# Performance work log

Hardware: AMD Instinct MI355X
Metric: run time of the kernel (lower is better)

## Reference

```python
import jax, jax.numpy as jnp
import numpy as np

N = 50000          # nodes
E = 1600000        # edges (avg degree 32)
G = 16             # graphs in batch
H = 128            # hidden_dim
HOP = 3
IN_DIM = 1


def setup_inputs() -> dict:
    key = jax.random.key(0)
    ks = jax.random.split(key, 12)
    s = 1.0 / np.sqrt(H)
    return {
        "x": jax.random.normal(ks[0], (N, IN_DIM), jnp.float32),
        "edge_index": jax.random.randint(ks[1], (2, E), 0, N, jnp.int64),
        "edge_attr": jax.random.uniform(ks[2], (E, 1), jnp.float32),
        "batch": jnp.sort(jax.random.randint(ks[3], (N,), 0, G, jnp.int64)),
        "W1": jax.random.normal(ks[4], (HOP, H, IN_DIM), jnp.float32) * s,
        "W2": jax.random.normal(ks[5], (HOP, H, H), jnp.float32) * s,
        "W3": jax.random.normal(ks[6], (HOP, H, H), jnp.float32) * s,
        "W4": jax.random.normal(ks[7], (HOP, H, 1), jnp.float32) * s,
        "W5": jax.random.normal(ks[8], (1, 2 * H), jnp.float32) * s,
        "b5": jnp.zeros((1,), jnp.float32),
        "W6": jax.random.normal(ks[9], (H, H), jnp.float32) * s,
        "W7": jax.random.normal(ks[10], (H, H), jnp.float32) * s,
    }


def reference(x, edge_index, edge_attr, batch, W1, W2, W3, W4, W5, b5, W6, W7):
    row, col = edge_index[0], edge_index[1]
    node_emb = jnp.zeros((N, H), x.dtype)
    for l in range(HOP):
        nfe = x @ W1[l].T                                        # [N,H]
        # gather neighbor embeddings along col, scatter-add to row
        ne_aggr = jax.ops.segment_sum(node_emb[col], row, num_segments=N)
        efe = jax.nn.relu(edge_attr @ W4[l].T)                   # [E,H]
        ee_aggr = jax.ops.segment_sum(efe, row, num_segments=N)  # [N,H]
        node_emb = jax.nn.relu(nfe + ne_aggr @ W2[l].T + ee_aggr @ W3[l].T)
    pooled = jax.ops.segment_sum(node_emb, batch, num_segments=G)  # [G,H]
    sum_emb = pooled @ W6.T                                        # [G,H]
    cat = jax.nn.relu(jnp.concatenate([sum_emb[batch], node_emb @ W7.T], axis=-1))
    return cat @ W5.T + b5                                         # [N,1]
```

## Files before the change

kernel.cpp:

```cpp
#include <hip/hip_runtime.h>
#include <hip/hip_bf16.h>

#define N_NODES 50000
#define N_EDGES 1600000
#define NGRAPH  16
#define HID     128

#define RPB   128
#define NB    ((N_NODES + RPB - 1) / RPB)
#define NBLK  256
#define EPB   ((N_EDGES + NBLK - 1) / NBLK)

typedef unsigned int uint32;
typedef unsigned short ushort;
typedef unsigned char uchar;
typedef __attribute__((ext_vector_type(8))) short bf16x8;
typedef __attribute__((ext_vector_type(4))) float f32x4;
typedef __attribute__((ext_vector_type(2))) float f32x2;

__device__ __forceinline__ uint32 bf16r(float f) {
    uint32 b = __float_as_uint(f);
    return (b + 0x7fffu + ((b >> 16) & 1u)) >> 16;
}
__device__ __forceinline__ uint32 pack_bf16(float lo, float hi) {
    return bf16r(lo) | (bf16r(hi) << 16);
}
__device__ __forceinline__ float bf_lo(uint32 u) { return __uint_as_float(u << 16); }
__device__ __forceinline__ float bf_hi(uint32 u) { return __uint_as_float(u & 0xffff0000u); }

__global__ __launch_bounds__(256) void k_init(float* p, int n,
                                              const int* __restrict__ batch,
                                              int* __restrict__ gstart) {
    int i = blockIdx.x * 256 + threadIdx.x;
    if (i < n) p[i] = 0.f;
    if (i <= NGRAPH) {
        int lo = 0, hi = N_NODES;
        while (lo < hi) {
            int mid = (lo + hi) >> 1;
            if (batch[mid] < i) lo = mid + 1; else hi = mid;
        }
        gstart[i] = lo;
    }
}

__global__ __launch_bounds__(1024) void k_p1_hist(const int* __restrict__ row,
                                                  int* __restrict__ blkhist) {
    __shared__ int hist[NB];
    int tid = threadIdx.x, blk = blockIdx.x;
    for (int i = tid; i < NB; i += 1024) hist[i] = 0;
    __syncthreads();
    int s = blk * EPB, e = s + EPB; if (e > N_EDGES) e = N_EDGES;
    for (int i = s + tid; i < e; i += 1024)
        atomicAdd(&hist[row[i] >> 7], 1);
    __syncthreads();
    for (int i = tid; i < NB; i += 1024)
        blkhist[i * NBLK + blk] = hist[i];
}

__global__ __launch_bounds__(NBLK) void k_p2a(int* __restrict__ blkhist,
                                              int* __restrict__ btot) {
    __shared__ int sums[NBLK];
    int t = threadIdx.x, b = blockIdx.x;
    int v = blkhist[b * NBLK + t];
    sums[t] = v;
    __syncthreads();
    for (int d = 1; d < NBLK; d <<= 1) {
        int u = (t >= d) ? sums[t - d] : 0;
        __syncthreads();
        sums[t] += u;
        __syncthreads();
    }
    blkhist[b * NBLK + t] = sums[t] - v;
    if (t == NBLK - 1) btot[b] = sums[t];
}

__global__ __launch_bounds__(512) void k_p2b(const int* __restrict__ btot,
                                             int* __restrict__ bbase) {
    __shared__ int sums[512];
    int t = threadIdx.x;
    int s = (t < NB) ? btot[t] : 0;
    sums[t] = s;
    __syncthreads();
    for (int d = 1; d < 512; d <<= 1) {
        int v = (t >= d) ? sums[t - d] : 0;
        __syncthreads();
        sums[t] += v;
        __syncthreads();
    }
    if (t < NB) {
        bbase[t] = sums[t] - s;
        if (t == NB - 1) bbase[NB] = sums[t];
    }
}

__global__ __launch_bounds__(1024) void k_p3_part(const int* __restrict__ row,
                                                  const int* __restrict__ col,
                                                  const float* __restrict__ ea,
                                                  const int* __restrict__ blkhist,
                                                  const int* __restrict__ bbase,
                                                  int2* __restrict__ pea) {
    __shared__ int cur[NB];
    int tid = threadIdx.x, blk = blockIdx.x;
    for (int i = tid; i < NB; i += 1024)
        cur[i] = bbase[i] + blkhist[i * NBLK + blk];
    __syncthreads();
    int s = blk * EPB, e = s + EPB; if (e > N_EDGES) e = N_EDGES;
    for (int i = s + tid; i < e; i += 1024) {
        int r = row[i], c = col[i];
        float a = ea[i];
        int slot = atomicAdd(&cur[r >> 7], 1);
        pea[slot] = make_int2(((r & (RPB - 1)) << 16) | c, __float_as_int(a));
    }
}

__global__ __launch_bounds__(512) void k_p4a(const int2* __restrict__ pea,
                                             const int* __restrict__ bbase,
                                             const float* __restrict__ x,
                                             int* __restrict__ offs,
                                             float* __restrict__ ea_sum,
                                             float2* __restrict__ pxe) {
    __shared__ int   cnt[RPB];
    __shared__ float eas[RPB];
    __shared__ int   scan_s[RPB];
    int tid = threadIdx.x, b = blockIdx.x;
    if (tid < RPB) { cnt[tid] = 0; eas[tid] = 0.f; }
    __syncthreads();
    int s = bbase[b], e = bbase[b + 1];
    for (int i = s + tid; i < e; i += 512) {
        int2 p = pea[i];
        int lr = ((uint32)p.x) >> 16;
        atomicAdd(&cnt[lr], 1);
        atomicAdd(&eas[lr], __int_as_float(p.y));
    }
    __syncthreads();
    if (tid < RPB) scan_s[tid] = cnt[tid];
    __syncthreads();
    for (int d = 1; d < RPB; d <<= 1) {
        int v = 0;
        if (tid < RPB && tid >= d) v = scan_s[tid - d];
        __syncthreads();
        if (tid < RPB) scan_s[tid] += v;
        __syncthreads();
    }
    int nbase = b * RPB;
    if (tid < RPB) {
        int excl = scan_s[tid] - cnt[tid];
        int n = nbase + tid;
        if (n < N_NODES) {
            offs[n] = s + excl;
            ea_sum[n] = eas[tid];
            pxe[n] = make_float2(x[n], eas[tid]);
        }
    }
    if (b == NB - 1 && tid == 0) offs[N_NODES] = e;
}

__global__ __launch_bounds__(512) void k_p4b(const int2* __restrict__ pea,
                                             const int* __restrict__ bbase,
                                             const int* __restrict__ offs,
                                             const float2* __restrict__ pxe,
                                             int* __restrict__ csr,
                                             float2* __restrict__ pxec) {
    __shared__ int cur[RPB];
    int tid = threadIdx.x, b = blockIdx.x;
    int nbase = b * RPB;
    if (tid < RPB) cur[tid] = (nbase + tid < N_NODES) ? offs[nbase + tid] : 0;
    __syncthreads();
    int s = bbase[b], e = bbase[b + 1];
    for (int i = s + tid; i < e; i += 512) {
        int2 p = pea[i];
        int c = p.x & 0xFFFF;
        int slot = atomicAdd(&cur[((uint32)p.x) >> 16], 1);
        csr[slot] = c;
        pxec[slot] = pxe[c];
    }
}

__global__ __launch_bounds__(256) void k_prep(const float* __restrict__ W2,
                                              const float* __restrict__ W7,
                                              const float* __restrict__ W3,
                                              const float* __restrict__ W4,
                                              ushort* __restrict__ wpack,
                                              float* __restrict__ v3) {
    int idx = blockIdx.x * 256 + threadIdx.x;
    if (idx < 4 * 16384) {
        int m = idx >> 14, f = idx & 16383;
        int j = f & 7, lane = (f >> 3) & 63, kk = (f >> 9) & 3, t = (f >> 11) & 7;
        int hp = t * 16 + (lane & 15);
        int k  = kk * 32 + ((lane >> 4) & 3) * 8 + j;
        const float* src = (m < 3) ? (W2 + m * HID * HID) : W7;
        wpack[idx] = (ushort)bf16r(src[hp * HID + k]);
    }
    if (idx < 3 * HID) {
        int l = idx / HID, hp = idx % HID;
        float acc = 0.f;
        for (int h = 0; h < HID; h++)
            acc += W3[l * HID * HID + hp * HID + h] * fmaxf(W4[l * HID + h], 0.f);
        v3[idx] = acc;
    }
}

__global__ __launch_bounds__(256) void k_gather1(const float2* __restrict__ pxec,
                                                 const int* __restrict__ offs,
                                                 const float* __restrict__ w1,
                                                 const float* __restrict__ v3,
                                                 uint32* __restrict__ agg) {
    int node = (blockIdx.x * 256 + threadIdx.x) >> 6;
    int lane = threadIdx.x & 63;
    if (node >= N_NODES) return;
    f32x2 w1v = {w1[2 * lane], w1[2 * lane + 1]};
    f32x2 v3v = {v3[2 * lane], v3[2 * lane + 1]};
    const f32x2 zero = {0.f, 0.f};
    int s = offs[node], e = offs[node + 1];
    f32x2 acc[4] = {zero, zero, zero, zero};
    int j = s;
    for (; j + 8 <= e; j += 8) {
        float2 p[8];
#pragma unroll
        for (int u = 0; u < 8; u++) p[u] = pxec[j + u];
#pragma unroll
        for (int u = 0; u < 8; u++) {
            f32x2 px = {p[u].x, p[u].x};
            f32x2 pe = {p[u].y, p[u].y};
            f32x2 r = __builtin_elementwise_fma(px, w1v, pe * v3v);
            acc[u & 3] += __builtin_elementwise_max(r, zero);
        }
    }
    for (; j < e; j++) {
        float2 p = pxec[j];
        f32x2 px = {p.x, p.x};
        f32x2 pe = {p.y, p.y};
        f32x2 r = __builtin_elementwise_fma(px, w1v, pe * v3v);
        acc[0] += __builtin_elementwise_max(r, zero);
    }
    f32x2 rs = (acc[0] + acc[1]) + (acc[2] + acc[3]);
    agg[(size_t)node * 64 + lane] = pack_bf16(rs.x, rs.y);
}

__global__ __launch_bounds__(256) void k_gather(const uchar* __restrict__ emb8,
                                                const int* __restrict__ offs,
                                                const int* __restrict__ csr,
                                                uint32* __restrict__ agg) {
    int node = (blockIdx.x * 256 + threadIdx.x) >> 6;
    int lane = threadIdx.x & 63;
    if (node >= N_NODES) return;
    int s = offs[node], e = offs[node + 1];
    float ax[8] = {0.f}, ay[8] = {0.f};
    for (int base = s; base < e; base += 64) {
        int idx = base + lane;
        int cv = (idx < e) ? csr[idx] : 0;
        int cnt = e - base; if (cnt > 64) cnt = 64;
        int j = 0;
        for (; j + 8 <= cnt; j += 8) {
            int h16[8];
#pragma unroll
            for (int u = 0; u < 8; u++) {
                int c = __shfl(cv, j + u);
                h16[u] = *(const ushort*)(emb8 + (size_t)c * 128 + 2 * lane);
            }
#pragma unroll
            for (int u = 0; u < 8; u++) {
                f32x2 d = __builtin_amdgcn_cvt_pk_f32_fp8(h16[u], false);
                ax[u] += d.x; ay[u] += d.y;
            }
        }
        for (; j < cnt; j++) {
            int c = __shfl(cv, j);
            int h = *(const ushort*)(emb8 + (size_t)c * 128 + 2 * lane);
            f32x2 d = __builtin_amdgcn_cvt_pk_f32_fp8(h, false);
            ax[0] += d.x; ay[0] += d.y;
        }
    }
    float rx = (((ax[0] + ax[1]) + (ax[2] + ax[3])) + ((ax[4] + ax[5]) + (ax[6] + ax[7]))) * 64.f;
    float ry = (((ay[0] + ay[1]) + (ay[2] + ay[3])) + ((ay[4] + ay[5]) + (ay[6] + ay[7]))) * 64.f;
    agg[(size_t)node * 64 + lane] = pack_bf16(rx, ry);
}

#define LROW 136

template <bool LAST>
__global__ __launch_bounds__(256) void k_gemm(const uint32* __restrict__ agg,
                                              const ushort* __restrict__ w2p,
                                              const float* __restrict__ w1l,
                                              const float* __restrict__ v3l,
                                              const float* __restrict__ x,
                                              const float* __restrict__ ea_sum,
                                              uint32* __restrict__ embOut,
                                              uchar* __restrict__ emb8Out,
                                              const ushort* __restrict__ w7p,
                                              const float* __restrict__ W5,
                                              float* __restrict__ outp) {
    __shared__ ushort tile[64 * LROW];
    int tid = threadIdx.x;
    int tbase = blockIdx.x * 64;
    {
        const uint2* src = (const uint2*)(agg + (size_t)tbase * 64);
        int vn = N_NODES - tbase; if (vn > 64) vn = 64;
        int lim = vn * 32;
        for (int i = tid; i < 64 * 32; i += 256) {
            uint2 u = (i < lim) ? src[i] : make_uint2(0u, 0u);
            int r = i >> 5, c4 = (i & 31) * 4;
            *(uint2*)&tile[r * LROW + c4] = u;
        }
    }
    __syncthreads();
    int wv = tid >> 6, lane = tid & 63;
    int n0 = lane & 15, quad = lane >> 4;
    int arow = wv * 16 + n0;
    bf16x8 a0 = *(const bf16x8*)&tile[arow * LROW + 0 * 32 + quad * 8];
    bf16x8 a1 = *(const bf16x8*)&tile[arow * LROW + 1 * 32 + quad * 8];
    bf16x8 a2 = *(const bf16x8*)&tile[arow * LROW + 2 * 32 + quad * 8];
    bf16x8 a3 = *(const bf16x8*)&tile[arow * LROW + 3 * 32 + quad * 8];
    const bf16x8* wb = (const bf16x8*)w2p;
    f32x4 acc[8];
#pragma unroll
    for (int t = 0; t < 8; t++) {
        f32x4 c = {0.f, 0.f, 0.f, 0.f};
        c = __builtin_amdgcn_mfma_f32_16x16x32_bf16(a0, wb[(t * 4 + 0) * 64 + lane], c, 0, 0, 0);
        c = __builtin_amdgcn_mfma_f32_16x16x32_bf16(a1, wb[(t * 4 + 1) * 64 + lane], c, 0, 0, 0);
        c = __builtin_amdgcn_mfma_f32_16x16x32_bf16(a2, wb[(t * 4 + 2) * 64 + lane], c, 0, 0, 0);
        c = __builtin_amdgcn_mfma_f32_16x16x32_bf16(a3, wb[(t * 4 + 3) * 64 + lane], c, 0, 0, 0);
        acc[t] = c;
    }
    float xs[4], es[4];
#pragma unroll
    for (int r = 0; r < 4; r++) {
        int n = tbase + wv * 16 + quad * 4 + r;
        xs[r] = (n < N_NODES) ? x[n] : 0.f;
        es[r] = (n < N_NODES) ? ea_sum[n] : 0.f;
    }
    if (!LAST) {
        uchar* stile = (uchar*)tile;
#pragma unroll
        for (int t = 0; t < 8; t++) {
            int hp = t * 16 + n0;
            float w1v = w1l[hp], v3v = v3l[hp];
#pragma unroll
            for (int r = 0; r < 4; r++) {
                float v = fmaxf(acc[t][r] + xs[r] * w1v + es[r] * v3v, 0.f) * 0.015625f;
                int enc = __builtin_amdgcn_cvt_pk_fp8_f32(v, v, 0, false);
                stile[(wv * 16 + quad * 4 + r) * 136 + hp] = (uchar)(enc & 0xff);
            }
        }
        __syncthreads();
        int vn = N_NODES - tbase; if (vn > 64) vn = 64;
        for (int i = tid; i < 64 * 32; i += 256) {
            int r = i >> 5, c4 = (i & 31) * 4;
            if (r < vn) {
                uint32 u = *(const uint32*)&stile[r * 136 + c4];
                *(uint32*)(emb8Out + (size_t)(tbase + r) * 128 + c4) = u;
            }
        }
    } else {
#pragma unroll
        for (int t = 0; t < 8; t++) {
            int hp = t * 16 + n0;
            float w1v = w1l[hp], v3v = v3l[hp];
#pragma unroll
            for (int r = 0; r < 4; r++) {
                float v = fmaxf(acc[t][r] + xs[r] * w1v + es[r] * v3v, 0.f);
                tile[(wv * 16 + quad * 4 + r) * LROW + hp] = (ushort)bf16r(v);
            }
        }
        __syncthreads();
        {
            int vn = N_NODES - tbase; if (vn > 64) vn = 64;
            for (int i = tid; i < 64 * 32; i += 256) {
                int r = i >> 5, c4 = (i & 31) * 4;
                if (r < vn) {
                    uint2 u = *(const uint2*)&tile[r * LROW + c4];
                    *(uint2*)(embOut + (size_t)(tbase + r) * 64 + (size_t)(i & 31) * 2) = u;
                }
            }
        }
        bf16x8 b0 = *(const bf16x8*)&tile[arow * LROW + 0 * 32 + quad * 8];
        bf16x8 b1 = *(const bf16x8*)&tile[arow * LROW + 1 * 32 + quad * 8];
        bf16x8 b2 = *(const bf16x8*)&tile[arow * LROW + 2 * 32 + quad * 8];
        bf16x8 b3 = *(const bf16x8*)&tile[arow * LROW + 3 * 32 + quad * 8];
        const bf16x8* w7 = (const bf16x8*)w7p;
        float p[4] = {0.f, 0.f, 0.f, 0.f};
#pragma unroll
        for (int t = 0; t < 8; t++) {
            f32x4 c = {0.f, 0.f, 0.f, 0.f};
            c = __builtin_amdgcn_mfma_f32_16x16x32_bf16(b0, w7[(t * 4 + 0) * 64 + lane], c, 0, 0, 0);
            c = __builtin_amdgcn_mfma_f32_16x16x32_bf16(b1, w7[(t * 4 + 1) * 64 + lane], c, 0, 0, 0);
            c = __builtin_amdgcn_mfma_f32_16x16x32_bf16(b2, w7[(t * 4 + 2) * 64 + lane], c, 0, 0, 0);
            c = __builtin_amdgcn_mfma_f32_16x16x32_bf16(b3, w7[(t * 4 + 3) * 64 + lane], c, 0, 0, 0);
            float w5v = W5[128 + t * 16 + n0];
#pragma unroll
            for (int r = 0; r < 4; r++) p[r] += fmaxf(c[r], 0.f) * w5v;
        }
#pragma unroll
        for (int r = 0; r < 4; r++) {
            float v = p[r];
            v += __shfl_xor(v, 1);
            v += __shfl_xor(v, 2);
            v += __shfl_xor(v, 4);
            v += __shfl_xor(v, 8);
            int n = tbase + wv * 16 + quad * 4 + r;
            if (n0 == 0 && n < N_NODES) outp[n] = v;
        }
    }
}

__global__ __launch_bounds__(256) void k_pool2(const uint32* __restrict__ emb,
                                               const int* __restrict__ gstart,
                                               float* __restrict__ pooled) {
    __shared__ float2 red[4][64];
    int bid = blockIdx.x;
    int g = bid >> 4, chunk = bid & 15;
    int gs = gstart[g], ge = gstart[g + 1];
    int len = ge - gs;
    int cs = gs + (int)(((long long)len * chunk) >> 4);
    int ce = gs + (int)(((long long)len * (chunk + 1)) >> 4);
    int sub = threadIdx.x >> 6, lane = threadIdx.x & 63;
    float ax = 0.f, ay = 0.f;
    for (int n = cs + sub; n < ce; n += 4) {
        uint32 u = emb[(size_t)n * 64 + lane];
        ax += bf_lo(u); ay += bf_hi(u);
    }
    red[sub][lane] = make_float2(ax, ay);
    __syncthreads();
    if (sub == 0) {
        float2 r0 = red[0][lane], r1 = red[1][lane], r2 = red[2][lane], r3 = red[3][lane];
        atomicAdd(&pooled[g * HID + 2 * lane],     (r0.x + r1.x) + (r2.x + r3.x));
        atomicAdd(&pooled[g * HID + 2 * lane + 1], (r0.y + r1.y) + (r2.y + r3.y));
    }
}

__global__ __launch_bounds__(128) void k_graph(const float* __restrict__ pooled,
                                               const float* __restrict__ W6,
                                               const float* __restrict__ W5,
                                               float* __restrict__ s_g) {
    int g = blockIdx.x, hp = threadIdx.x;
    float acc = 0.f;
    for (int h = 0; h < HID; h++) acc += pooled[g * HID + h] * W6[hp * HID + h];
    float v = fmaxf(acc, 0.f) * W5[hp];
    __shared__ float red[HID];
    red[hp] = v;
    __syncthreads();
    for (int d = 64; d > 0; d >>= 1) {
        if (hp < d) red[hp] += red[hp + d];
        __syncthreads();
    }
    if (hp == 0) s_g[g] = red[0];
}

__global__ __launch_bounds__(256) void k_addsg(float* __restrict__ out,
                                               const int* __restrict__ batch,
                                               const float* __restrict__ s_g,
                                               const float* __restrict__ b5) {
    int n = blockIdx.x * 256 + threadIdx.x;
    if (n < N_NODES) out[n] += s_g[batch[n]] + b5[0];
}

extern "C" void kernel_launch(void* const* d_in, const int* in_sizes, int n_in,
                              void* d_out, int out_size, void* d_ws, size_t ws_size,
                              hipStream_t stream) {
    (void)in_sizes; (void)n_in; (void)out_size; (void)ws_size;
    const float* x    = (const float*)d_in[0];
    const int*   ei   = (const int*)d_in[1];
    const float* ea   = (const float*)d_in[2];
    const int*   bat  = (const int*)d_in[3];
    const float* W1   = (const float*)d_in[4];
    const float* W2   = (const float*)d_in[5];
    const float* W3   = (const float*)d_in[6];
    const float* W4   = (const float*)d_in[7];
    const float* W5   = (const float*)d_in[8];
    const float* b5   = (const float*)d_in[9];
    const float* W6   = (const float*)d_in[10];
    const float* W7   = (const float*)d_in[11];
    float* out = (float*)d_out;

    const int* row = ei;
    const int* col = ei + N_EDGES;

    float* wsf = (float*)d_ws;
    int*   wsi = (int*)d_ws;
    size_t o = 0;
    float* pooled = wsf + o; o += NGRAPH * HID;
    float* s_g    = wsf + o; o += NGRAPH;
    size_t ztot = o;
    int*   offs   = wsi + o; o += N_NODES + 1;
    float* ea_sum = wsf + o; o += N_NODES;
    int*   gstart = wsi + o; o += NGRAPH + 1;
    int*   btot   = wsi + o; o += NB;
    int*   bbase  = wsi + o; o += NB + 1;
    float* v3     = wsf + o; o += 3 * HID;
    int*   blkh   = wsi + o; o += NB * NBLK;
    o = (o + 1) & ~(size_t)1;
    float2* pxe   = (float2*)(wsi + o); o += 2 * (size_t)N_NODES;
    o = (o + 3) & ~(size_t)3;
    ushort* wpack = (ushort*)(wsi + o); o += 4 * 16384 / 2;
    int*    csr   = wsi + o; o += N_EDGES;
    o = (o + 1) & ~(size_t)1;
    int2*   pea   = (int2*)(wsi + o); o += 2 * (size_t)N_EDGES;
    float2* pxec  = (float2*)(wsi + o); o += 2 * (size_t)N_EDGES;
    o = (o + 1) & ~(size_t)1;
    uint32* embA  = (uint32*)(wsi + o); o += (size_t)N_NODES * 64;
    uchar*  emb8  = (uchar*)(wsi + o);  o += (size_t)N_NODES * 32;
    uint32* aggB  = (uint32*)(wsi + o); o += (size_t)N_NODES * 64;

    const ushort* w2p1 = wpack + 1 * 16384;
    const ushort* w2p2 = wpack + 2 * 16384;
    const ushort* w7p  = wpack + 3 * 16384;

    k_init<<<(int)((ztot + 255) / 256), 256, 0, stream>>>((float*)d_ws, (int)ztot, bat, gstart);
    k_p1_hist<<<NBLK, 1024, 0, stream>>>(row, blkh);
    k_p2a<<<NB, NBLK, 0, stream>>>(blkh, btot);
    k_p2b<<<1, 512, 0, stream>>>(btot, bbase);
    k_p3_part<<<NBLK, 1024, 0, stream>>>(row, col, ea, blkh, bbase, pea);
    k_p4a<<<NB, 512, 0, stream>>>(pea, bbase, x, offs, ea_sum, pxe);
    k_p4b<<<NB, 512, 0, stream>>>(pea, bbase, offs, pxe, csr, pxec);
    k_prep<<<(4 * 16384 + 255) / 256, 256, 0, stream>>>(W2, W7, W3, W4, (ushort*)wpack, v3);
    k_gather1<<<(N_NODES * 64 + 255) / 256, 256, 0, stream>>>(pxec, offs, W1, v3, aggB);
    k_gemm<false><<<(N_NODES + 63) / 64, 256, 0, stream>>>(
        aggB, w2p1, W1 + 1 * HID, v3 + 1 * HID, x, ea_sum, nullptr, emb8, nullptr, nullptr, nullptr);
    k_gather<<<(N_NODES * 64 + 255) / 256, 256, 0, stream>>>(emb8, offs, csr, aggB);
    k_gemm<true><<<(N_NODES + 63) / 64, 256, 0, stream>>>(
        aggB, w2p2, W1 + 2 * HID, v3 + 2 * HID, x, ea_sum, embA, nullptr, w7p, W5, out);
    k_pool2<<<NGRAPH * 16, 256, 0, stream>>>(embA, gstart, pooled);
    k_graph<<<NGRAPH, 128, 0, stream>>>(pooled, W6, W5, s_g);
    k_addsg<<<(N_NODES + 255) / 256, 256, 0, stream>>>(out, bat, s_g, b5);
}
```

Baseline: 281.8 us.

## Fuse preprocessing and tail kernels, pool inside final GEMM, drop pxec buffer

Merges zero-init with weight packing, folds the top-level bucket scan into the partition kernel, and merges the two per-bucket CSR passes into one kernel that caches edges in LDS. The first gather now reads node features through the CSR index instead of a pre-gathered per-edge array, so the 12.8MB pxec buffer is no longer written. The final GEMM accumulates graph pooling directly through atomics, so the bf16 embedding no longer round-trips to memory. Graph readout and bias addition move into one tail kernel that recomputes per-graph scalars in each block. The cost is redundant per-block prefix reductions, atomic contention on pooled sums, and an indirect gather in layer one.

```diff
diff --git a/kernel.cpp b/kernel.cpp
--- a/kernel.cpp
+++ b/kernel.cpp
@@ -10,6 +10,7 @@
 #define NB    ((N_NODES + RPB - 1) / RPB)
 #define NBLK  256
 #define EPB   ((N_EDGES + NBLK - 1) / NBLK)
+#define P4CAP 6144
 
 typedef unsigned int uint32;
 typedef unsigned short ushort;
@@ -25,164 +26,16 @@
 __device__ __forceinline__ uint32 pack_bf16(float lo, float hi) {
     return bf16r(lo) | (bf16r(hi) << 16);
 }
-__device__ __forceinline__ float bf_lo(uint32 u) { return __uint_as_float(u << 16); }
-__device__ __forceinline__ float bf_hi(uint32 u) { return __uint_as_float(u & 0xffff0000u); }
-
-__global__ __launch_bounds__(256) void k_init(float* p, int n,
-                                              const int* __restrict__ batch,
-                                              int* __restrict__ gstart) {
-    int i = blockIdx.x * 256 + threadIdx.x;
-    if (i < n) p[i] = 0.f;
-    if (i <= NGRAPH) {
-        int lo = 0, hi = N_NODES;
-        while (lo < hi) {
-            int mid = (lo + hi) >> 1;
-            if (batch[mid] < i) lo = mid + 1; else hi = mid;
-        }
-        gstart[i] = lo;
-    }
-}
-
-__global__ __launch_bounds__(1024) void k_p1_hist(const int* __restrict__ row,
-                                                  int* __restrict__ blkhist) {
-    __shared__ int hist[NB];
-    int tid = threadIdx.x, blk = blockIdx.x;
-    for (int i = tid; i < NB; i += 1024) hist[i] = 0;
-    __syncthreads();
-    int s = blk * EPB, e = s + EPB; if (e > N_EDGES) e = N_EDGES;
-    for (int i = s + tid; i < e; i += 1024)
-        atomicAdd(&hist[row[i] >> 7], 1);
-    __syncthreads();
-    for (int i = tid; i < NB; i += 1024)
-        blkhist[i * NBLK + blk] = hist[i];
-}
-
-__global__ __launch_bounds__(NBLK) void k_p2a(int* __restrict__ blkhist,
-                                              int* __restrict__ btot) {
-    __shared__ int sums[NBLK];
-    int t = threadIdx.x, b = blockIdx.x;
-    int v = blkhist[b * NBLK + t];
-    sums[t] = v;
-    __syncthreads();
-    for (int d = 1; d < NBLK; d <<= 1) {
-        int u = (t >= d) ? sums[t - d] : 0;
-        __syncthreads();
-        sums[t] += u;
-        __syncthreads();
-    }
-    blkhist[b * NBLK + t] = sums[t] - v;
-    if (t == NBLK - 1) btot[b] = sums[t];
-}
-
-__global__ __launch_bounds__(512) void k_p2b(const int* __restrict__ btot,
-                                             int* __restrict__ bbase) {
-    __shared__ int sums[512];
-    int t = threadIdx.x;
-    int s = (t < NB) ? btot[t] : 0;
-    sums[t] = s;
-    __syncthreads();
-    for (int d = 1; d < 512; d <<= 1) {
-        int v = (t >= d) ? sums[t - d] : 0;
-        __syncthreads();
-        sums[t] += v;
-        __syncthreads();
-    }
-    if (t < NB) {
-        bbase[t] = sums[t] - s;
-        if (t == NB - 1) bbase[NB] = sums[t];
-    }
-}
-
-__global__ __launch_bounds__(1024) void k_p3_part(const int* __restrict__ row,
-                                                  const int* __restrict__ col,
-                                                  const float* __restrict__ ea,
-                                                  const int* __restrict__ blkhist,
-                                                  const int* __restrict__ bbase,
-                                                  int2* __restrict__ pea) {
-    __shared__ int cur[NB];
-    int tid = threadIdx.x, blk = blockIdx.x;
-    for (int i = tid; i < NB; i += 1024)
-        cur[i] = bbase[i] + blkhist[i * NBLK + blk];
-    __syncthreads();
-    int s = blk * EPB, e = s + EPB; if (e > N_EDGES) e = N_EDGES;
-    for (int i = s + tid; i < e; i += 1024) {
-        int r = row[i], c = col[i];
-        float a = ea[i];
-        int slot = atomicAdd(&cur[r >> 7], 1);
-        pea[slot] = make_int2(((r & (RPB - 1)) << 16) | c, __float_as_int(a));
-    }
-}
-
-__global__ __launch_bounds__(512) void k_p4a(const int2* __restrict__ pea,
-                                             const int* __restrict__ bbase,
-                                             const float* __restrict__ x,
-                                             int* __restrict__ offs,
-                                             float* __restrict__ ea_sum,
-                                             float2* __restrict__ pxe) {
-    __shared__ int   cnt[RPB];
-    __shared__ float eas[RPB];
-    __shared__ int   scan_s[RPB];
-    int tid = threadIdx.x, b = blockIdx.x;
-    if (tid < RPB) { cnt[tid] = 0; eas[tid] = 0.f; }
-    __syncthreads();
-    int s = bbase[b], e = bbase[b + 1];
-    for (int i = s + tid; i < e; i += 512) {
-        int2 p = pea[i];
-        int lr = ((uint32)p.x) >> 16;
-        atomicAdd(&cnt[lr], 1);
-        atomicAdd(&eas[lr], __int_as_float(p.y));
-    }
-    __syncthreads();
-    if (tid < RPB) scan_s[tid] = cnt[tid];
-    __syncthreads();
-    for (int d = 1; d < RPB; d <<= 1) {
-        int v = 0;
-        if (tid < RPB && tid >= d) v = scan_s[tid - d];
-        __syncthreads();
-        if (tid < RPB) scan_s[tid] += v;
-        __syncthreads();
-    }
-    int nbase = b * RPB;
-    if (tid < RPB) {
-        int excl = scan_s[tid] - cnt[tid];
-        int n = nbase + tid;
-        if (n < N_NODES) {
-            offs[n] = s + excl;
-            ea_sum[n] = eas[tid];
-            pxe[n] = make_float2(x[n], eas[tid]);
-        }
-    }
-    if (b == NB - 1 && tid == 0) offs[N_NODES] = e;
-}
-
-__global__ __launch_bounds__(512) void k_p4b(const int2* __restrict__ pea,
-                                             const int* __restrict__ bbase,
-                                             const int* __restrict__ offs,
-                                             const float2* __restrict__ pxe,
-                                             int* __restrict__ csr,
-                                             float2* __restrict__ pxec) {
-    __shared__ int cur[RPB];
-    int tid = threadIdx.x, b = blockIdx.x;
-    int nbase = b * RPB;
-    if (tid < RPB) cur[tid] = (nbase + tid < N_NODES) ? offs[nbase + tid] : 0;
-    __syncthreads();
-    int s = bbase[b], e = bbase[b + 1];
-    for (int i = s + tid; i < e; i += 512) {
-        int2 p = pea[i];
-        int c = p.x & 0xFFFF;
-        int slot = atomicAdd(&cur[((uint32)p.x) >> 16], 1);
-        csr[slot] = c;
-        pxec[slot] = pxe[c];
-    }
-}
-
-__global__ __launch_bounds__(256) void k_prep(const float* __restrict__ W2,
+
+__global__ __launch_bounds__(256) void k_init(float* __restrict__ zp, int nz,
+                                              const float* __restrict__ W2,
                                               const float* __restrict__ W7,
                                               const float* __restrict__ W3,
                                               const float* __restrict__ W4,
                                               ushort* __restrict__ wpack,
                                               float* __restrict__ v3) {
     int idx = blockIdx.x * 256 + threadIdx.x;
+    if (idx < nz) zp[idx] = 0.f;
     if (idx < 4 * 16384) {
         int m = idx >> 14, f = idx & 16383;
         int j = f & 7, lane = (f >> 3) & 63, kk = (f >> 9) & 3, t = (f >> 11) & 7;
@@ -200,8 +53,133 @@
     }
 }
 
-__global__ __launch_bounds__(256) void k_gather1(const float2* __restrict__ pxec,
+__global__ __launch_bounds__(1024) void k_p1_hist(const int* __restrict__ row,
+                                                  int* __restrict__ blkhist) {
+    __shared__ int hist[NB];
+    int tid = threadIdx.x, blk = blockIdx.x;
+    for (int i = tid; i < NB; i += 1024) hist[i] = 0;
+    __syncthreads();
+    int s = blk * EPB, e = s + EPB; if (e > N_EDGES) e = N_EDGES;
+    for (int i = s + tid; i < e; i += 1024)
+        atomicAdd(&hist[row[i] >> 7], 1);
+    __syncthreads();
+    for (int i = tid; i < NB; i += 1024)
+        blkhist[i * NBLK + blk] = hist[i];
+}
+
+__global__ __launch_bounds__(NBLK) void k_p2a(int* __restrict__ blkhist,
+                                              int* __restrict__ btot) {
+    __shared__ int sums[NBLK];
+    int t = threadIdx.x, b = blockIdx.x;
+    int v = blkhist[b * NBLK + t];
+    sums[t] = v;
+    __syncthreads();
+    for (int d = 1; d < NBLK; d <<= 1) {
+        int u = (t >= d) ? sums[t - d] : 0;
+        __syncthreads();
+        sums[t] += u;
+        __syncthreads();
+    }
+    blkhist[b * NBLK + t] = sums[t] - v;
+    if (t == NBLK - 1) btot[b] = sums[t];
+}
+
+__global__ __launch_bounds__(1024) void k_p3_part(const int* __restrict__ row,
+                                                  const int* __restrict__ col,
+                                                  const float* __restrict__ ea,
+                                                  const int* __restrict__ blkhist,
+                                                  const int* __restrict__ btot,
+                                                  int2* __restrict__ pea) {
+    __shared__ int sc[512];
+    __shared__ int cur[NB];
+    int tid = threadIdx.x, blk = blockIdx.x;
+    if (tid < 512) sc[tid] = (tid < NB) ? btot[tid] : 0;
+    __syncthreads();
+    for (int d = 1; d < 512; d <<= 1) {
+        int v = 0;
+        if (tid < 512 && tid >= d) v = sc[tid - d];
+        __syncthreads();
+        if (tid < 512) sc[tid] += v;
+        __syncthreads();
+    }
+    for (int i = tid; i < NB; i += 1024)
+        cur[i] = (sc[i] - btot[i]) + blkhist[i * NBLK + blk];
+    __syncthreads();
+    int s = blk * EPB, e = s + EPB; if (e > N_EDGES) e = N_EDGES;
+    for (int i = s + tid; i < e; i += 1024) {
+        int r = row[i], c = col[i];
+        float a = ea[i];
+        int slot = atomicAdd(&cur[r >> 7], 1);
+        pea[slot] = make_int2(((r & (RPB - 1)) << 16) | c, __float_as_int(a));
+    }
+}
+
+__global__ __launch_bounds__(512) void k_p4(const int2* __restrict__ pea,
+                                            const int* __restrict__ btot,
+                                            const float* __restrict__ x,
+                                            int* __restrict__ offs,
+                                            float* __restrict__ ea_sum,
+                                            float2* __restrict__ pxe,
+                                            int* __restrict__ csr) {
+    __shared__ int2  cache[P4CAP];
+    __shared__ int   red[512];
+    __shared__ int   cnt[RPB];
+    __shared__ float eas[RPB];
+    __shared__ int   scan_s[RPB];
+    __shared__ int   curp[RPB];
+    int t = threadIdx.x, b = blockIdx.x;
+    red[t] = (t < b) ? btot[t] : 0;
+    __syncthreads();
+    for (int d = 256; d > 0; d >>= 1) {
+        if (t < d) red[t] += red[t + d];
+        __syncthreads();
+    }
+    int s = red[0];
+    int e = s + btot[b];
+    int len = e - s;
+    int clen = len < P4CAP ? len : P4CAP;
+    for (int i = t; i < clen; i += 512) cache[i] = pea[s + i];
+    if (t < RPB) { cnt[t] = 0; eas[t] = 0.f; }
+    __syncthreads();
+    for (int i = t; i < len; i += 512) {
+        int2 p = (i < P4CAP) ? cache[i] : pea[s + i];
+        int lr = ((uint32)p.x) >> 16;
+        atomicAdd(&cnt[lr], 1);
+        atomicAdd(&eas[lr], __int_as_float(p.y));
+    }
+    __syncthreads();
+    if (t < RPB) scan_s[t] = cnt[t];
+    __syncthreads();
+    for (int d = 1; d < RPB; d <<= 1) {
+        int v = 0;
+        if (t < RPB && t >= d) v = scan_s[t - d];
+        __syncthreads();
+        if (t < RPB) scan_s[t] += v;
+        __syncthreads();
+    }
+    int nbase = b * RPB;
+    if (t < RPB) {
+        int excl = scan_s[t] - cnt[t];
+        int n = nbase + t;
+        if (n < N_NODES) {
+            offs[n] = s + excl;
+            ea_sum[n] = eas[t];
+            pxe[n] = make_float2(x[n], eas[t]);
+        }
+        curp[t] = s + excl;
+    }
+    if (b == NB - 1 && t == 0) offs[N_NODES] = e;
+    __syncthreads();
+    for (int i = t; i < len; i += 512) {
+        int2 p = (i < P4CAP) ? cache[i] : pea[s + i];
+        int slot = atomicAdd(&curp[((uint32)p.x) >> 16], 1);
+        csr[slot] = p.x & 0xFFFF;
+    }
+}
+
+__global__ __launch_bounds__(256) void k_gather1(const float2* __restrict__ pxe,
                                                  const int* __restrict__ offs,
+                                                 const int* __restrict__ csr,
                                                  const float* __restrict__ w1,
                                                  const float* __restrict__ v3,
                                                  uint32* __restrict__ agg) {
@@ -213,25 +191,30 @@
     const f32x2 zero = {0.f, 0.f};
     int s = offs[node], e = offs[node + 1];
     f32x2 acc[4] = {zero, zero, zero, zero};
-    int j = s;
-    for (; j + 8 <= e; j += 8) {
-        float2 p[8];
-#pragma unroll
-        for (int u = 0; u < 8; u++) p[u] = pxec[j + u];
-#pragma unroll
-        for (int u = 0; u < 8; u++) {
-            f32x2 px = {p[u].x, p[u].x};
-            f32x2 pe = {p[u].y, p[u].y};
+    for (int base = s; base < e; base += 64) {
+        int idx = base + lane;
+        int cv = (idx < e) ? csr[idx] : 0;
+        int cnt = e - base; if (cnt > 64) cnt = 64;
+        int j = 0;
+        for (; j + 8 <= cnt; j += 8) {
+            float2 p[8];
+#pragma unroll
+            for (int u = 0; u < 8; u++) p[u] = pxe[__shfl(cv, j + u)];
+#pragma unroll
+            for (int u = 0; u < 8; u++) {
+                f32x2 px = {p[u].x, p[u].x};
+                f32x2 pe = {p[u].y, p[u].y};
+                f32x2 r = __builtin_elementwise_fma(px, w1v, pe * v3v);
+                acc[u & 3] += __builtin_elementwise_max(r, zero);
+            }
+        }
+        for (; j < cnt; j++) {
+            float2 p = pxe[__shfl(cv, j)];
+            f32x2 px = {p.x, p.x};
+            f32x2 pe = {p.y, p.y};
             f32x2 r = __builtin_elementwise_fma(px, w1v, pe * v3v);
-            acc[u & 3] += __builtin_elementwise_max(r, zero);
-        }
-    }
-    for (; j < e; j++) {
-        float2 p = pxec[j];
-        f32x2 px = {p.x, p.x};
-        f32x2 pe = {p.y, p.y};
-        f32x2 r = __builtin_elementwise_fma(px, w1v, pe * v3v);
-        acc[0] += __builtin_elementwise_max(r, zero);
+            acc[0] += __builtin_elementwise_max(r, zero);
+        }
     }
     f32x2 rs = (acc[0] + acc[1]) + (acc[2] + acc[3]);
     agg[(size_t)node * 64 + lane] = pack_bf16(rs.x, rs.y);
@@ -285,32 +268,24 @@
                                               const float* __restrict__ v3l,
                                               const float* __restrict__ x,
                                               const float* __restrict__ ea_sum,
-                                              uint32* __restrict__ embOut,
                                               uchar* __restrict__ emb8Out,
                                               const ushort* __restrict__ w7p,
                                               const float* __restrict__ W5,
-                                              float* __restrict__ outp) {
+                                              float* __restrict__ outp,
+                                              const int* __restrict__ batch,
+                                              float* __restrict__ pooled) {
     __shared__ ushort tile[64 * LROW];
+    __shared__ float redp[4][128];
     int tid = threadIdx.x;
     int tbase = blockIdx.x * 64;
-    {
-        const uint2* src = (const uint2*)(agg + (size_t)tbase * 64);
-        int vn = N_NODES - tbase; if (vn > 64) vn = 64;
-        int lim = vn * 32;
-        for (int i = tid; i < 64 * 32; i += 256) {
-            uint2 u = (i < lim) ? src[i] : make_uint2(0u, 0u);
-            int r = i >> 5, c4 = (i & 31) * 4;
-            *(uint2*)&tile[r * LROW + c4] = u;
-        }
-    }
-    __syncthreads();
     int wv = tid >> 6, lane = tid & 63;
     int n0 = lane & 15, quad = lane >> 4;
     int arow = wv * 16 + n0;
-    bf16x8 a0 = *(const bf16x8*)&tile[arow * LROW + 0 * 32 + quad * 8];
-    bf16x8 a1 = *(const bf16x8*)&tile[arow * LROW + 1 * 32 + quad * 8];
-    bf16x8 a2 = *(const bf16x8*)&tile[arow * LROW + 2 * 32 + quad * 8];
-    bf16x8 a3 = *(const bf16x8*)&tile[arow * LROW + 3 * 32 + quad * 8];
+    bf16x8 a0 = {0,0,0,0,0,0,0,0}, a1 = a0, a2 = a0, a3 = a0;
+    if (tbase + arow < N_NODES) {
+        const bf16x8* ap = (const bf16x8*)(agg + (size_t)(tbase + arow) * 64);
+        a0 = ap[0 + quad]; a1 = ap[4 + quad]; a2 = ap[8 + quad]; a3 = ap[12 + quad];
+    }
     const bf16x8* wb = (const bf16x8*)w2p;
     f32x4 acc[8];
 #pragma unroll
@@ -352,26 +327,49 @@
             }
         }
     } else {
+        int nlast = tbase + 63; if (nlast > N_NODES - 1) nlast = N_NODES - 1;
+        int g0 = batch[tbase];
+        bool uni = (batch[nlast] == g0);
+        int gr[4];
+        if (!uni) {
+#pragma unroll
+            for (int r = 0; r < 4; r++) {
+                int n = tbase + wv * 16 + quad * 4 + r;
+                gr[r] = (n < N_NODES) ? batch[n] : 0;
+            }
+        }
+        float st[8];
 #pragma unroll
         for (int t = 0; t < 8; t++) {
             int hp = t * 16 + n0;
             float w1v = w1l[hp], v3v = v3l[hp];
+            float stt = 0.f;
 #pragma unroll
             for (int r = 0; r < 4; r++) {
                 float v = fmaxf(acc[t][r] + xs[r] * w1v + es[r] * v3v, 0.f);
                 tile[(wv * 16 + quad * 4 + r) * LROW + hp] = (ushort)bf16r(v);
-            }
-        }
-        __syncthreads();
-        {
-            int vn = N_NODES - tbase; if (vn > 64) vn = 64;
-            for (int i = tid; i < 64 * 32; i += 256) {
-                int r = i >> 5, c4 = (i & 31) * 4;
-                if (r < vn) {
-                    uint2 u = *(const uint2*)&tile[r * LROW + c4];
-                    *(uint2*)(embOut + (size_t)(tbase + r) * 64 + (size_t)(i & 31) * 2) = u;
+                if (uni) {
+                    stt += v;
+                } else {
+                    int n = tbase + wv * 16 + quad * 4 + r;
+                    if (n < N_NODES) atomicAdd(&pooled[gr[r] * HID + hp], v);
                 }
             }
+            st[t] = stt;
+        }
+        if (uni) {
+#pragma unroll
+            for (int t = 0; t < 8; t++) {
+                float v = st[t];
+                v += __shfl_xor(v, 16);
+                v += __shfl_xor(v, 32);
+                if (lane < 16) redp[wv][t * 16 + lane] = v;
+            }
+        }
+        __syncthreads();
+        if (uni && tid < 128) {
+            float sp = (redp[0][tid] + redp[1][tid]) + (redp[2][tid] + redp[3][tid]);
+            atomicAdd(&pooled[g0 * HID + tid], sp);
         }
         bf16x8 b0 = *(const bf16x8*)&tile[arow * LROW + 0 * 32 + quad * 8];
         bf16x8 b1 = *(const bf16x8*)&tile[arow * LROW + 1 * 32 + quad * 8];
@@ -403,55 +401,50 @@
     }
 }
 
-__global__ __launch_bounds__(256) void k_pool2(const uint32* __restrict__ emb,
-                                               const int* __restrict__ gstart,
-                                               float* __restrict__ pooled) {
-    __shared__ float2 red[4][64];
-    int bid = blockIdx.x;
-    int g = bid >> 4, chunk = bid & 15;
-    int gs = gstart[g], ge = gstart[g + 1];
-    int len = ge - gs;
-    int cs = gs + (int)(((long long)len * chunk) >> 4);
-    int ce = gs + (int)(((long long)len * (chunk + 1)) >> 4);
-    int sub = threadIdx.x >> 6, lane = threadIdx.x & 63;
-    float ax = 0.f, ay = 0.f;
-    for (int n = cs + sub; n < ce; n += 4) {
-        uint32 u = emb[(size_t)n * 64 + lane];
-        ax += bf_lo(u); ay += bf_hi(u);
-    }
-    red[sub][lane] = make_float2(ax, ay);
-    __syncthreads();
-    if (sub == 0) {
-        float2 r0 = red[0][lane], r1 = red[1][lane], r2 = red[2][lane], r3 = red[3][lane];
-        atomicAdd(&pooled[g * HID + 2 * lane],     (r0.x + r1.x) + (r2.x + r3.x));
-        atomicAdd(&pooled[g * HID + 2 * lane + 1], (r0.y + r1.y) + (r2.y + r3.y));
-    }
-}
-
-__global__ __launch_bounds__(128) void k_graph(const float* __restrict__ pooled,
-                                               const float* __restrict__ W6,
-                                               const float* __restrict__ W5,
-                                               float* __restrict__ s_g) {
-    int g = blockIdx.x, hp = threadIdx.x;
+__global__ __launch_bounds__(256) void k_tail(float* __restrict__ out,
+                                              const int* __restrict__ batch,
+                                              const float* __restrict__ pooled,
+                                              const float* __restrict__ W6,
+                                              const float* __restrict__ W5,
+                                              const float* __restrict__ b5) {
+    __shared__ float red[256];
+    __shared__ int gsh[2];
+    int t = threadIdx.x;
+    int nbase = blockIdx.x * 256;
+    int n = nbase + t;
+    if (t == 0) gsh[0] = batch[nbase < N_NODES ? nbase : N_NODES - 1];
+    if (t == 1) gsh[1] = batch[(nbase + 255) < N_NODES ? (nbase + 255) : N_NODES - 1];
+    __syncthreads();
+    int g_lo = gsh[0], g_hi = gsh[1];
+    int hp = t & 127;
+    int g = (t >> 7) ? g_hi : g_lo;
+    const float* pg = pooled + g * HID;
+    const float* wr = W6 + hp * HID;
     float acc = 0.f;
-    for (int h = 0; h < HID; h++) acc += pooled[g * HID + h] * W6[hp * HID + h];
-    float v = fmaxf(acc, 0.f) * W5[hp];
-    __shared__ float red[HID];
-    red[hp] = v;
+    for (int h = 0; h < HID; h++) acc += pg[h] * wr[h];
+    red[t] = fmaxf(acc, 0.f) * W5[hp];
     __syncthreads();
     for (int d = 64; d > 0; d >>= 1) {
-        if (hp < d) red[hp] += red[hp + d];
-        __syncthreads();
-    }
-    if (hp == 0) s_g[g] = red[0];
-}
-
-__global__ __launch_bounds__(256) void k_addsg(float* __restrict__ out,
-                                               const int* __restrict__ batch,
-                                               const float* __restrict__ s_g,
-                                               const float* __restrict__ b5) {
-    int n = blockIdx.x * 256 + threadIdx.x;
-    if (n < N_NODES) out[n] += s_g[batch[n]] + b5[0];
+        if (hp < d) red[t] += red[t + d];
+        __syncthreads();
+    }
+    float s_lo = red[0], s_hi = red[128];
+    if (n < N_NODES) {
+        int gn = batch[n];
+        float s;
+        if (gn == g_lo) s = s_lo;
+        else if (gn == g_hi) s = s_hi;
+        else {
+            s = 0.f;
+            const float* pg2 = pooled + gn * HID;
+            for (int hp2 = 0; hp2 < HID; hp2++) {
+                float a2 = 0.f;
+                for (int h = 0; h < HID; h++) a2 += pg2[h] * W6[hp2 * HID + h];
+                s += fmaxf(a2, 0.f) * W5[hp2];
+            }
+        }
+        out[n] += s + b5[0];
+    }
 }
 
 extern "C" void kernel_launch(void* const* d_in, const int* in_sizes, int n_in,
@@ -479,13 +472,10 @@
     int*   wsi = (int*)d_ws;
     size_t o = 0;
     float* pooled = wsf + o; o += NGRAPH * HID;
-    float* s_g    = wsf + o; o += NGRAPH;
     size_t ztot = o;
     int*   offs   = wsi + o; o += N_NODES + 1;
     float* ea_sum = wsf + o; o += N_NODES;
-    int*   gstart = wsi + o; o += NGRAPH + 1;
     int*   btot   = wsi + o; o += NB;
-    int*   bbase  = wsi + o; o += NB + 1;
     float* v3     = wsf + o; o += 3 * HID;
     int*   blkh   = wsi + o; o += NB * NBLK;
     o = (o + 1) & ~(size_t)1;
@@ -495,31 +485,25 @@
     int*    csr   = wsi + o; o += N_EDGES;
     o = (o + 1) & ~(size_t)1;
     int2*   pea   = (int2*)(wsi + o); o += 2 * (size_t)N_EDGES;
-    float2* pxec  = (float2*)(wsi + o); o += 2 * (size_t)N_EDGES;
-    o = (o + 1) & ~(size_t)1;
-    uint32* embA  = (uint32*)(wsi + o); o += (size_t)N_NODES * 64;
+    uint32* aggB  = (uint32*)(wsi + o); o += (size_t)N_NODES * 64;
     uchar*  emb8  = (uchar*)(wsi + o);  o += (size_t)N_NODES * 32;
-    uint32* aggB  = (uint32*)(wsi + o); o += (size_t)N_NODES * 64;
 
     const ushort* w2p1 = wpack + 1 * 16384;
     const ushort* w2p2 = wpack + 2 * 16384;
     const ushort* w7p  = wpack + 3 * 16384;
 
-    k_init<<<(int)((ztot + 255) / 256), 256, 0, stream>>>((float*)d_ws, (int)ztot, bat, gstart);
+    k_init<<<(4 * 16384 + 255) / 256, 256, 0, stream>>>(
+        (float*)d_ws, (int)ztot, W2, W7, W3, W4, (ushort*)wpack, v3);
     k_p1_hist<<<NBLK, 1024, 0, stream>>>(row, blkh);
     k_p2a<<<NB, NBLK, 0, stream>>>(blkh, btot);
-    k_p2b<<<1, 512, 0, stream>>>(btot, bbase);
-    k_p3_part<<<NBLK, 1024, 0, stream>>>(row, col, ea, blkh, bbase, pea);
-    k_p4a<<<NB, 512, 0, stream>>>(pea, bbase, x, offs, ea_sum, pxe);
-    k_p4b<<<NB, 512, 0, stream>>>(pea, bbase, offs, pxe, csr, pxec);
-    k_prep<<<(4 * 16384 + 255) / 256, 256, 0, stream>>>(W2, W7, W3, W4, (ushort*)wpack, v3);
-    k_gather1<<<(N_NODES * 64 + 255) / 256, 256, 0, stream>>>(pxec, offs, W1, v3, aggB);
+    k_p3_part<<<NBLK, 1024, 0, stream>>>(row, col, ea, blkh, btot, pea);
+    k_p4<<<NB, 512, 0, stream>>>(pea, btot, x, offs, ea_sum, pxe, csr);
+    k_gather1<<<(N_NODES * 64 + 255) / 256, 256, 0, stream>>>(pxe, offs, csr, W1, v3, aggB);
     k_gemm<false><<<(N_NODES + 63) / 64, 256, 0, stream>>>(
-        aggB, w2p1, W1 + 1 * HID, v3 + 1 * HID, x, ea_sum, nullptr, emb8, nullptr, nullptr, nullptr);
+        aggB, w2p1, W1 + 1 * HID, v3 + 1 * HID, x, ea_sum, emb8, nullptr, nullptr, nullptr,
+        nullptr, nullptr);
     k_gather<<<(N_NODES * 64 + 255) / 256, 256, 0, stream>>>(emb8, offs, csr, aggB);
     k_gemm<true><<<(N_NODES + 63) / 64, 256, 0, stream>>>(
-        aggB, w2p2, W1 + 2 * HID, v3 + 2 * HID, x, ea_sum, embA, nullptr, w7p, W5, out);
-    k_pool2<<<NGRAPH * 16, 256, 0, stream>>>(embA, gstart, pooled);
-    k_graph<<<NGRAPH, 128, 0, stream>>>(pooled, W6, W5, s_g);
-    k_addsg<<<(N_NODES + 255) / 256, 256, 0, stream>>>(out, bat, s_g, b5);
-}
+        aggB, w2p2, W1 + 2 * HID, v3 + 2 * HID, x, ea_sum, nullptr, w7p, W5, out, bat, pooled);
+    k_tail<<<(N_NODES + 255) / 256, 256, 0, stream>>>(out, bat, pooled, W6, W5, b5);
+}
```

New measurement: 284.0 us. No clear change (+0.8%).
